# Kernel optimization log

Measured on AMD Instinct MI355X. Metric: run time of the kernel, lower is better.

Reference implementation:

```python
import jax, jax.numpy as jnp
import numpy as np

B, H, W = 32, 512, 512


def setup_inputs() -> dict:
    key = jax.random.key(0)
    k1, k2, k3 = jax.random.split(key, 3)
    pred = jax.random.uniform(k1, (B, 2, H, W), dtype=jnp.float32)
    # so the topk hard-negative-mining branch is exercised
    r1 = jax.random.uniform(k2, (B, H, W), dtype=jnp.float32)
    r2 = jax.random.uniform(k3, (B, H, W), dtype=jnp.float32)
    region_scores = jnp.where(r1 > 0.9, r1, 0.0)
    affinity_scores = jnp.where(r2 > 0.9, r2, 0.0)
    return {"pred": pred, "region_scores": region_scores, "affinity_scores": affinity_scores}


def _ohem_sum(pre_loss, label):
    """Vectorized equivalent of single_image_loss: returns sum over batch of per-sample OHEM loss.
    pre_loss, label: [B, N] float32."""
    b, n = pre_loss.shape
    pos = label >= 0.1                               # [B, N] bool
    pos_cnt = pos.sum(axis=-1)                       # [B] int
    neg_cnt = n - pos_cnt
    # mean over positive pixels
    posi_loss = jnp.where(pos, pre_loss, 0.0).sum(axis=-1) / jnp.maximum(pos_cnt, 1)
    # negatives sorted descending (positives pushed to the end with -1 < any mse loss... mse >= 0)
    neg_vals = jnp.where(pos, -1.0, pre_loss)
    neg_sorted = -jnp.sort(-neg_vals, axis=-1)       # [B, N] descending, negatives first
    csum = jnp.cumsum(neg_sorted, axis=-1)
    # k = min(3*pos_cnt, neg_cnt): mean of all negatives if fewer than 3*pos, else top-3*pos
    k = jnp.minimum(3 * pos_cnt, neg_cnt)            # [B]
    idx = jnp.clip(k - 1, 0, n - 1)
    nega_loss = jnp.take_along_axis(csum, idx[:, None], axis=-1)[:, 0] / jnp.maximum(k, 1)
    # fallback when no positive pixels: mean of top-500 losses over the whole image
    top500 = jax.lax.top_k(pre_loss, 500)[0].mean(axis=-1)
    per_sample = jnp.where(pos_cnt > 0, posi_loss + nega_loss, top500)
    return per_sample.sum()


def reference(pred, region_scores, affinity_scores):
    b = pred.shape[0]
    p_gh = pred[:, 0, :, :]
    p_gah = pred[:, 1, :, :]
    loss1 = (p_gh - region_scores) ** 2              # MSELoss(reduction='none')
    loss2 = (p_gah - affinity_scores) ** 2
    char_loss = _ohem_sum(loss1.reshape(b, -1), region_scores.reshape(b, -1))
    affi_loss = _ohem_sum(loss2.reshape(b, -1), affinity_scores.reshape(b, -1))
    return char_loss / b + affi_loss / b
```

## Files before the change

### kernel.cpp

```cpp
#include <hip/hip_runtime.h>


#define NB 2048
#define HSTRIDE 2056
#define NPIX 262144
#define C_CHUNKS 8
#define CHUNK (NPIX / C_CHUNKS)
#define SCALE 1048576.0f
#define INV_SCALE (1.0 / 1048576.0)

__global__ __launch_bounds__(1024)
void ohem_hist_kernel(const float* __restrict__ pred,
                      const float* __restrict__ region,
                      const float* __restrict__ affinity,
                      unsigned long long* __restrict__ g_hist)
{
    __shared__ unsigned long long h[NB + 1];
    const int row   = blockIdx.x / C_CHUNKS;
    const int chunk = blockIdx.x % C_CHUNKS;
    const int b = row & 31;
    const int c = row >> 5;
    const float* p = pred + (size_t)(b * 2 + c) * NPIX + (size_t)chunk * CHUNK;
    const float* s = (c == 0 ? region : affinity) + (size_t)b * NPIX + (size_t)chunk * CHUNK;

    for (int i = threadIdx.x; i <= NB; i += 1024) h[i] = 0;
    __syncthreads();

    const float4* p4 = (const float4*)p;
    const float4* s4 = (const float4*)s;
    #pragma unroll
    for (int it = 0; it < CHUNK / 4096; ++it) {
        float4 pv = p4[it * 1024 + threadIdx.x];
        float4 sv = s4[it * 1024 + threadIdx.x];
        float pp[4]  = {pv.x, pv.y, pv.z, pv.w};
        float ssv[4] = {sv.x, sv.y, sv.z, sv.w};
        #pragma unroll
        for (int j = 0; j < 4; ++j) {
            float d = pp[j] - ssv[j];
            float x = d * d;
            int bin;
            if (ssv[j] >= 0.1f) {
                bin = NB;
            } else {
                bin = (int)(x * (float)NB);
                if (bin > NB - 1) bin = NB - 1;
            }
            unsigned long long packed =
                (1ULL << 40) | (unsigned long long)(x * SCALE + 0.5f);
            atomicAdd(&h[bin], packed);
        }
    }
    __syncthreads();

    unsigned long long* gh = g_hist + (size_t)row * HSTRIDE;
    for (int i = threadIdx.x; i <= NB; i += 1024) {
        unsigned long long v = h[i];
        if (v) atomicAdd(&gh[i], v);
    }
}

__global__ __launch_bounds__(64)
void ohem_select_kernel(const unsigned long long* __restrict__ g_hist,
                        float* __restrict__ row_result)
{
    const int row = blockIdx.x;
    const unsigned long long* gh = g_hist + (size_t)row * HSTRIDE;
    const int t = threadIdx.x;
    const unsigned long long MASK = (1ULL << 40) - 1;

    unsigned long long c_t = 0, s_t = 0;
    for (int j = 0; j < 32; ++j) {
        int bin = NB - 1 - (t * 32 + j);
        unsigned long long v = gh[bin];
        c_t += v >> 40;
        s_t += v & MASK;
    }
    unsigned long long ic = c_t, isum = s_t;
    for (int off = 1; off < 64; off <<= 1) {
        unsigned long long uc = __shfl_up(ic, off);
        unsigned long long us = __shfl_up(isum, off);
        if (t >= off) { ic += uc; isum += us; }
    }
    unsigned long long pre_c = ic - c_t;
    unsigned long long pre_s = isum - s_t;

    unsigned long long pospack = gh[NB];
    unsigned long long pc = pospack >> 40;
    double psum = (double)(pospack & MASK) * INV_SCALE;
    long long negc = (long long)NPIX - (long long)pc;
    long long k;
    if (pc > 0) { k = 3LL * (long long)pc; if (k > negc) k = negc; }
    else        { k = 500; }

    if (pc > 0 && k == 0) {
        if (t == 0) row_result[row] = (float)(psum / (double)pc - 1.0);
        return;
    }

    if ((long long)pre_c < k && k <= (long long)(pre_c + c_t)) {
        unsigned long long cum = pre_c, cums = pre_s;
        double nega = 0.0;
        for (int j = 0; j < 32; ++j) {
            int bin = NB - 1 - (t * 32 + j);
            unsigned long long v = gh[bin];
            unsigned long long cb = v >> 40, sb = v & MASK;
            if ((long long)(cum + cb) >= k) {
                unsigned long long need = (unsigned long long)k - cum;
                double avg = cb ? (double)sb / (double)cb : 0.0;
                nega = ((double)cums + (double)need * avg) * INV_SCALE / (double)k;
                break;
            }
            cum += cb; cums += sb;
        }
        double posi = (pc > 0) ? psum / (double)pc : 0.0;
        row_result[row] = (float)(posi + nega);
    }
}

__global__ void final_reduce_kernel(const float* __restrict__ row_result,
                                    float* __restrict__ out)
{
    float v = row_result[threadIdx.x];
    #pragma unroll
    for (int off = 32; off > 0; off >>= 1) v += __shfl_down(v, off);
    if (threadIdx.x == 0) out[0] = v * (1.0f / 32.0f);
}

extern "C" void kernel_launch(void* const* d_in, const int* in_sizes, int n_in,
                              void* d_out, int out_size, void* d_ws, size_t ws_size,
                              hipStream_t stream)
{
    const float* pred     = (const float*)d_in[0];
    const float* region   = (const float*)d_in[1];
    const float* affinity = (const float*)d_in[2];
    float* out = (float*)d_out;

    unsigned long long* g_hist = (unsigned long long*)d_ws;
    const size_t hist_bytes = (size_t)64 * HSTRIDE * sizeof(unsigned long long);
    float* row_result = (float*)((char*)d_ws + hist_bytes);

    hipMemsetAsync(d_ws, 0, hist_bytes + 64 * sizeof(float), stream);
    ohem_hist_kernel<<<64 * C_CHUNKS, 1024, 0, stream>>>(pred, region, affinity, g_hist);
    ohem_select_kernel<<<64, 64, 0, stream>>>(g_hist, row_result);
    final_reduce_kernel<<<1, 64, 0, stream>>>(row_result, out);
}
```

Measured before the change: 40.81 us.

## Use 32-bit count-only histogram with bin-midpoint sums and separate positive reduction

```diff
diff --git a/kernel.cpp b/kernel.cpp
--- a/kernel.cpp
+++ b/kernel.cpp
@@ -2,91 +2,99 @@
 
 
 #define NB 2048
-#define HSTRIDE 2056
+#define ROWSTRIDE 2080
 #define NPIX 262144
-#define C_CHUNKS 8
+#define C_CHUNKS 16
+#define BLK 512
 #define CHUNK (NPIX / C_CHUNKS)
 #define SCALE 1048576.0f
 #define INV_SCALE (1.0 / 1048576.0)
 
-__global__ __launch_bounds__(1024)
+__global__ __launch_bounds__(BLK)
 void ohem_hist_kernel(const float* __restrict__ pred,
                       const float* __restrict__ region,
                       const float* __restrict__ affinity,
-                      unsigned long long* __restrict__ g_hist)
+                      unsigned int* __restrict__ g_hist,
+                      unsigned long long* __restrict__ g_pos)
 {
-    __shared__ unsigned long long h[NB + 1];
+    __shared__ unsigned int h[NB];
     const int row   = blockIdx.x / C_CHUNKS;
     const int chunk = blockIdx.x % C_CHUNKS;
     const int b = row & 31;
     const int c = row >> 5;
-    const float* p = pred + (size_t)(b * 2 + c) * NPIX + (size_t)chunk * CHUNK;
-    const float* s = (c == 0 ? region : affinity) + (size_t)b * NPIX + (size_t)chunk * CHUNK;
+    const float4* p4 = (const float4*)(pred + (size_t)(b * 2 + c) * NPIX
+                                            + (size_t)chunk * CHUNK);
+    const float4* s4 = (const float4*)((c == 0 ? region : affinity)
+                                       + (size_t)b * NPIX + (size_t)chunk * CHUNK);
 
-    for (int i = threadIdx.x; i <= NB; i += 1024) h[i] = 0;
+    for (int i = threadIdx.x; i < NB; i += BLK) h[i] = 0;
     __syncthreads();
 
-    const float4* p4 = (const float4*)p;
-    const float4* s4 = (const float4*)s;
+    unsigned int poscnt = 0, possum = 0;
     #pragma unroll
-    for (int it = 0; it < CHUNK / 4096; ++it) {
-        float4 pv = p4[it * 1024 + threadIdx.x];
-        float4 sv = s4[it * 1024 + threadIdx.x];
+    for (int it = 0; it < CHUNK / (BLK * 4); ++it) {
+        float4 pv = p4[it * BLK + threadIdx.x];
+        float4 sv = s4[it * BLK + threadIdx.x];
         float pp[4]  = {pv.x, pv.y, pv.z, pv.w};
-        float ssv[4] = {sv.x, sv.y, sv.z, sv.w};
+        float ss[4]  = {sv.x, sv.y, sv.z, sv.w};
         #pragma unroll
         for (int j = 0; j < 4; ++j) {
-            float d = pp[j] - ssv[j];
+            float d = pp[j] - ss[j];
             float x = d * d;
-            int bin;
-            if (ssv[j] >= 0.1f) {
-                bin = NB;
+            if (ss[j] >= 0.1f) {
+                poscnt += 1;
+                possum += (unsigned int)(x * SCALE + 0.5f);
             } else {
-                bin = (int)(x * (float)NB);
+                int bin = (int)(x * (float)NB);
                 if (bin > NB - 1) bin = NB - 1;
+                atomicAdd(&h[bin], 1u);
             }
-            unsigned long long packed =
-                (1ULL << 40) | (unsigned long long)(x * SCALE + 0.5f);
-            atomicAdd(&h[bin], packed);
         }
     }
+
+    unsigned long long pp64 = ((unsigned long long)poscnt << 40)
+                            | (unsigned long long)possum;
+    #pragma unroll
+    for (int off = 32; off > 0; off >>= 1) pp64 += __shfl_down(pp64, off);
+    if ((threadIdx.x & 63) == 0 && pp64) atomicAdd(&g_pos[row], pp64);
+
     __syncthreads();
-
-    unsigned long long* gh = g_hist + (size_t)row * HSTRIDE;
-    for (int i = threadIdx.x; i <= NB; i += 1024) {
-        unsigned long long v = h[i];
+    unsigned int* gh = g_hist + (size_t)row * ROWSTRIDE;
+    for (int i = threadIdx.x; i < NB; i += BLK) {
+        unsigned int v = h[i];
         if (v) atomicAdd(&gh[i], v);
     }
 }
 
 __global__ __launch_bounds__(64)
-void ohem_select_kernel(const unsigned long long* __restrict__ g_hist,
+void ohem_select_kernel(const unsigned int* __restrict__ g_hist,
+                        const unsigned long long* __restrict__ g_pos,
                         float* __restrict__ row_result)
 {
     const int row = blockIdx.x;
-    const unsigned long long* gh = g_hist + (size_t)row * HSTRIDE;
+    const unsigned int* gh = g_hist + (size_t)row * ROWSTRIDE;
     const int t = threadIdx.x;
-    const unsigned long long MASK = (1ULL << 40) - 1;
 
-    unsigned long long c_t = 0, s_t = 0;
+    unsigned long long c_t = 0;
+    double w_t = 0.0;
     for (int j = 0; j < 32; ++j) {
         int bin = NB - 1 - (t * 32 + j);
-        unsigned long long v = gh[bin];
-        c_t += v >> 40;
-        s_t += v & MASK;
+        unsigned int v = gh[bin];
+        c_t += v;
+        w_t += (double)v * ((double)bin + 0.5);
     }
-    unsigned long long ic = c_t, isum = s_t;
+    unsigned long long ic = c_t; double iw = w_t;
     for (int off = 1; off < 64; off <<= 1) {
         unsigned long long uc = __shfl_up(ic, off);
-        unsigned long long us = __shfl_up(isum, off);
-        if (t >= off) { ic += uc; isum += us; }
+        double             uw = __shfl_up(iw, off);
+        if (t >= off) { ic += uc; iw += uw; }
     }
     unsigned long long pre_c = ic - c_t;
-    unsigned long long pre_s = isum - s_t;
+    double pre_w = iw - w_t;
 
-    unsigned long long pospack = gh[NB];
+    unsigned long long pospack = g_pos[row];
     unsigned long long pc = pospack >> 40;
-    double psum = (double)(pospack & MASK) * INV_SCALE;
+    double psum = (double)(pospack & ((1ULL << 40) - 1)) * INV_SCALE;
     long long negc = (long long)NPIX - (long long)pc;
     long long k;
     if (pc > 0) { k = 3LL * (long long)pc; if (k > negc) k = negc; }
@@ -98,19 +106,20 @@
     }
 
     if ((long long)pre_c < k && k <= (long long)(pre_c + c_t)) {
-        unsigned long long cum = pre_c, cums = pre_s;
+        unsigned long long cum = pre_c;
+        double cw = pre_w;
         double nega = 0.0;
         for (int j = 0; j < 32; ++j) {
             int bin = NB - 1 - (t * 32 + j);
-            unsigned long long v = gh[bin];
-            unsigned long long cb = v >> 40, sb = v & MASK;
-            if ((long long)(cum + cb) >= k) {
+            unsigned int v = gh[bin];
+            if ((long long)(cum + v) >= k) {
                 unsigned long long need = (unsigned long long)k - cum;
-                double avg = cb ? (double)sb / (double)cb : 0.0;
-                nega = ((double)cums + (double)need * avg) * INV_SCALE / (double)k;
+                nega = (cw + (double)need * ((double)bin + 0.5))
+                       / (double)NB / (double)k;
                 break;
             }
-            cum += cb; cums += sb;
+            cum += v;
+            cw  += (double)v * ((double)bin + 0.5);
         }
         double posi = (pc > 0) ? psum / (double)pc : 0.0;
         row_result[row] = (float)(posi + nega);
@@ -135,12 +144,16 @@
     const float* affinity = (const float*)d_in[2];
     float* out = (float*)d_out;
 
-    unsigned long long* g_hist = (unsigned long long*)d_ws;
-    const size_t hist_bytes = (size_t)64 * HSTRIDE * sizeof(unsigned long long);
-    float* row_result = (float*)((char*)d_ws + hist_bytes);
+    unsigned int* g_hist = (unsigned int*)d_ws;
+    const size_t hist_bytes = (size_t)64 * ROWSTRIDE * sizeof(unsigned int);
+    unsigned long long* g_pos = (unsigned long long*)((char*)d_ws + hist_bytes);
+    float* row_result = (float*)((char*)d_ws + hist_bytes + 64 * sizeof(unsigned long long));
 
-    hipMemsetAsync(d_ws, 0, hist_bytes + 64 * sizeof(float), stream);
-    ohem_hist_kernel<<<64 * C_CHUNKS, 1024, 0, stream>>>(pred, region, affinity, g_hist);
-    ohem_select_kernel<<<64, 64, 0, stream>>>(g_hist, row_result);
+    hipMemsetAsync(d_ws, 0,
+                   hist_bytes + 64 * sizeof(unsigned long long) + 64 * sizeof(float),
+                   stream);
+    ohem_hist_kernel<<<64 * C_CHUNKS, BLK, 0, stream>>>(pred, region, affinity,
+                                                        g_hist, g_pos);
+    ohem_select_kernel<<<64, 64, 0, stream>>>(g_hist, g_pos, row_result);
     final_reduce_kernel<<<1, 64, 0, stream>>>(row_result, out);
 }
```

Result: slower. 62.71 us (+53.7%).

## Bin by |d| with fewer bins and fuse select with final reduce

Applied to the files above, without the earlier changes.

```diff
diff --git a/kernel.cpp b/kernel.cpp
--- a/kernel.cpp
+++ b/kernel.cpp
@@ -1,15 +1,18 @@
 #include <hip/hip_runtime.h>
 
 
-#define NB 2048
-#define HSTRIDE 2056
+#define NB 1024
+#define BPL (NB / 64)
+#define RSTR 1032
 #define NPIX 262144
+#define NROWS 64
 #define C_CHUNKS 8
+#define BLK 1024
 #define CHUNK (NPIX / C_CHUNKS)
 #define SCALE 1048576.0f
 #define INV_SCALE (1.0 / 1048576.0)
 
-__global__ __launch_bounds__(1024)
+__global__ __launch_bounds__(BLK)
 void ohem_hist_kernel(const float* __restrict__ pred,
                       const float* __restrict__ region,
                       const float* __restrict__ affinity,
@@ -20,31 +23,30 @@
     const int chunk = blockIdx.x % C_CHUNKS;
     const int b = row & 31;
     const int c = row >> 5;
-    const float* p = pred + (size_t)(b * 2 + c) * NPIX + (size_t)chunk * CHUNK;
-    const float* s = (c == 0 ? region : affinity) + (size_t)b * NPIX + (size_t)chunk * CHUNK;
+    const float4* p4 = (const float4*)(pred + (size_t)(b * 2 + c) * NPIX
+                                            + (size_t)chunk * CHUNK);
+    const float4* s4 = (const float4*)((c == 0 ? region : affinity)
+                                       + (size_t)b * NPIX + (size_t)chunk * CHUNK);
 
-    for (int i = threadIdx.x; i <= NB; i += 1024) h[i] = 0;
+    h[threadIdx.x] = 0;
+    if (threadIdx.x == 0) h[NB] = 0;
     __syncthreads();
 
-    const float4* p4 = (const float4*)p;
-    const float4* s4 = (const float4*)s;
     #pragma unroll
-    for (int it = 0; it < CHUNK / 4096; ++it) {
-        float4 pv = p4[it * 1024 + threadIdx.x];
-        float4 sv = s4[it * 1024 + threadIdx.x];
-        float pp[4]  = {pv.x, pv.y, pv.z, pv.w};
-        float ssv[4] = {sv.x, sv.y, sv.z, sv.w};
+    for (int it = 0; it < 4; ++it) {
+        float4 pv0 = p4[(2 * it + 0) * BLK + threadIdx.x];
+        float4 sv0 = s4[(2 * it + 0) * BLK + threadIdx.x];
+        float4 pv1 = p4[(2 * it + 1) * BLK + threadIdx.x];
+        float4 sv1 = s4[(2 * it + 1) * BLK + threadIdx.x];
+        float pp[8] = {pv0.x, pv0.y, pv0.z, pv0.w, pv1.x, pv1.y, pv1.z, pv1.w};
+        float ss[8] = {sv0.x, sv0.y, sv0.z, sv0.w, sv1.x, sv1.y, sv1.z, sv1.w};
         #pragma unroll
-        for (int j = 0; j < 4; ++j) {
-            float d = pp[j] - ssv[j];
+        for (int j = 0; j < 8; ++j) {
+            float d = pp[j] - ss[j];
             float x = d * d;
-            int bin;
-            if (ssv[j] >= 0.1f) {
-                bin = NB;
-            } else {
-                bin = (int)(x * (float)NB);
-                if (bin > NB - 1) bin = NB - 1;
-            }
+            int bin = (int)(fabsf(d) * (float)NB);
+            if (bin > NB - 1) bin = NB - 1;
+            bin = (ss[j] >= 0.1f) ? NB : bin;
             unsigned long long packed =
                 (1ULL << 40) | (unsigned long long)(x * SCALE + 0.5f);
             atomicAdd(&h[bin], packed);
@@ -52,78 +54,83 @@
     }
     __syncthreads();
 
-    unsigned long long* gh = g_hist + (size_t)row * HSTRIDE;
-    for (int i = threadIdx.x; i <= NB; i += 1024) {
-        unsigned long long v = h[i];
-        if (v) atomicAdd(&gh[i], v);
+    unsigned long long* gh = g_hist + (size_t)row * RSTR;
+    unsigned long long v = h[threadIdx.x];
+    if (v) atomicAdd(&gh[threadIdx.x], v);
+    if (threadIdx.x == 0) {
+        unsigned long long pv = h[NB];
+        if (pv) atomicAdd(&gh[NB], pv);
     }
 }
 
-__global__ __launch_bounds__(64)
-void ohem_select_kernel(const unsigned long long* __restrict__ g_hist,
-                        float* __restrict__ row_result)
+__global__ __launch_bounds__(1024)
+void ohem_select_final_kernel(const unsigned long long* __restrict__ g_hist,
+                              float* __restrict__ out)
 {
-    const int row = blockIdx.x;
-    const unsigned long long* gh = g_hist + (size_t)row * HSTRIDE;
-    const int t = threadIdx.x;
+    __shared__ float rres[NROWS];
+    const int wave = threadIdx.x >> 6;
+    const int t    = threadIdx.x & 63;
     const unsigned long long MASK = (1ULL << 40) - 1;
 
-    unsigned long long c_t = 0, s_t = 0;
-    for (int j = 0; j < 32; ++j) {
-        int bin = NB - 1 - (t * 32 + j);
-        unsigned long long v = gh[bin];
-        c_t += v >> 40;
-        s_t += v & MASK;
-    }
-    unsigned long long ic = c_t, isum = s_t;
-    for (int off = 1; off < 64; off <<= 1) {
-        unsigned long long uc = __shfl_up(ic, off);
-        unsigned long long us = __shfl_up(isum, off);
-        if (t >= off) { ic += uc; isum += us; }
-    }
-    unsigned long long pre_c = ic - c_t;
-    unsigned long long pre_s = isum - s_t;
+    for (int row = wave * 4; row < wave * 4 + 4; ++row) {
+        const unsigned long long* gh = g_hist + (size_t)row * RSTR;
 
-    unsigned long long pospack = gh[NB];
-    unsigned long long pc = pospack >> 40;
-    double psum = (double)(pospack & MASK) * INV_SCALE;
-    long long negc = (long long)NPIX - (long long)pc;
-    long long k;
-    if (pc > 0) { k = 3LL * (long long)pc; if (k > negc) k = negc; }
-    else        { k = 500; }
+        unsigned long long c_t = 0, s_t = 0;
+        #pragma unroll
+        for (int j = 0; j < BPL; ++j) {
+            unsigned long long v = gh[NB - 1 - (t * BPL + j)];
+            c_t += v >> 40;
+            s_t += v & MASK;
+        }
+        unsigned long long ic = c_t, isum = s_t;
+        for (int off = 1; off < 64; off <<= 1) {
+            unsigned long long uc = __shfl_up(ic, off);
+            unsigned long long us = __shfl_up(isum, off);
+            if (t >= off) { ic += uc; isum += us; }
+        }
+        unsigned long long pre_c = ic - c_t;
+        unsigned long long pre_s = isum - s_t;
 
-    if (pc > 0 && k == 0) {
-        if (t == 0) row_result[row] = (float)(psum / (double)pc - 1.0);
-        return;
+        unsigned long long pospack = gh[NB];
+        unsigned long long pc = pospack >> 40;
+        double psum = (double)(pospack & MASK) * INV_SCALE;
+        long long negc = (long long)NPIX - (long long)pc;
+        long long k;
+        if (pc > 0) { k = 3LL * (long long)pc; if (k > negc) k = negc; }
+        else        { k = 500; }
+
+        if (pc > 0 && k == 0) {
+            if (t == 0) rres[row] = (float)(psum / (double)pc - 1.0);
+            continue;
+        }
+
+        if ((long long)pre_c < k && k <= (long long)(pre_c + c_t)) {
+            unsigned long long cum = pre_c, cums = pre_s;
+            double nega = 0.0;
+            for (int j = 0; j < BPL; ++j) {
+                unsigned long long v = gh[NB - 1 - (t * BPL + j)];
+                unsigned long long cb = v >> 40, sb = v & MASK;
+                if ((long long)(cum + cb) >= k) {
+                    unsigned long long need = (unsigned long long)k - cum;
+                    double avg = cb ? (double)sb / (double)cb : 0.0;
+                    nega = ((double)cums + (double)need * avg) * INV_SCALE
+                           / (double)k;
+                    break;
+                }
+                cum += cb; cums += sb;
+            }
+            double posi = (pc > 0) ? psum / (double)pc : 0.0;
+            rres[row] = (float)(posi + nega);
+        }
     }
 
-    if ((long long)pre_c < k && k <= (long long)(pre_c + c_t)) {
-        unsigned long long cum = pre_c, cums = pre_s;
-        double nega = 0.0;
-        for (int j = 0; j < 32; ++j) {
-            int bin = NB - 1 - (t * 32 + j);
-            unsigned long long v = gh[bin];
-            unsigned long long cb = v >> 40, sb = v & MASK;
-            if ((long long)(cum + cb) >= k) {
-                unsigned long long need = (unsigned long long)k - cum;
-                double avg = cb ? (double)sb / (double)cb : 0.0;
-                nega = ((double)cums + (double)need * avg) * INV_SCALE / (double)k;
-                break;
-            }
-            cum += cb; cums += sb;
-        }
-        double posi = (pc > 0) ? psum / (double)pc : 0.0;
-        row_result[row] = (float)(posi + nega);
+    __syncthreads();
+    if (threadIdx.x < 64) {
+        float v = rres[threadIdx.x];
+        #pragma unroll
+        for (int off = 32; off > 0; off >>= 1) v += __shfl_down(v, off);
+        if (threadIdx.x == 0) out[0] = v * (1.0f / 32.0f);
     }
-}
-
-__global__ void final_reduce_kernel(const float* __restrict__ row_result,
-                                    float* __restrict__ out)
-{
-    float v = row_result[threadIdx.x];
-    #pragma unroll
-    for (int off = 32; off > 0; off >>= 1) v += __shfl_down(v, off);
-    if (threadIdx.x == 0) out[0] = v * (1.0f / 32.0f);
 }
 
 extern "C" void kernel_launch(void* const* d_in, const int* in_sizes, int n_in,
@@ -136,11 +143,10 @@
     float* out = (float*)d_out;
 
     unsigned long long* g_hist = (unsigned long long*)d_ws;
-    const size_t hist_bytes = (size_t)64 * HSTRIDE * sizeof(unsigned long long);
-    float* row_result = (float*)((char*)d_ws + hist_bytes);
+    const size_t hist_bytes = (size_t)NROWS * RSTR * sizeof(unsigned long long);
 
-    hipMemsetAsync(d_ws, 0, hist_bytes + 64 * sizeof(float), stream);
-    ohem_hist_kernel<<<64 * C_CHUNKS, 1024, 0, stream>>>(pred, region, affinity, g_hist);
-    ohem_select_kernel<<<64, 64, 0, stream>>>(g_hist, row_result);
-    final_reduce_kernel<<<1, 64, 0, stream>>>(row_result, out);
+    hipMemsetAsync(d_ws, 0, hist_bytes, stream);
+    ohem_hist_kernel<<<NROWS * C_CHUNKS, BLK, 0, stream>>>(pred, region,
+                                                           affinity, g_hist);
+    ohem_select_final_kernel<<<1, 1024, 0, stream>>>(g_hist, out);
 }
```

After: 56.51 us. +38.5%, slower.
